# Kernel optimization log

Measured on AMD Instinct MI355X. Metric: run time of the kernel, lower is better.

The kernel has to match this reference:

```python
import jax, jax.numpy as jnp
import numpy as np
import math

PSIZE = [(8, 8), (16, 16)]


def _conv2d(x, w, b):
    # 3x3 stride-1 'SAME' conv, NCHW / OIHW
    y = jax.lax.conv_general_dilated(
        x, w, window_strides=(1, 1), padding='SAME',
        dimension_numbers=('NCHW', 'OIHW', 'NCHW'))
    return y + b[None, :, None, None]


def _patch_attention(x, xs, b, t, c, h, w, ph, pw):
    oh, ow = h // ph, w // pw
    d = c * ph * pw
    # query: [b, oh*ow, c*ph*pw]
    q = x.reshape(b, c, oh, ph, ow, pw).transpose(0, 2, 4, 1, 3, 5).reshape(b, oh * ow, d)
    # key/value: [b, t*oh*ow, c*ph*pw]
    k = xs.reshape(b, t, c, oh, ph, ow, pw).transpose(0, 1, 3, 5, 2, 4, 6).reshape(b, t * oh * ow, d)
    scores = jnp.einsum('bqd,bkd->bqk', q, k) / jnp.asarray(math.sqrt(d), x.dtype)
    # NOTE: the original torch code calls scores.masked_fill(mm, -1e9) without
    # assigning the result, so the mask has NO effect; we faithfully omit it.
    atten = jax.nn.softmax(scores, axis=-1)
    val = jnp.einsum('bqk,bkd->bqd', atten, k)
    y = val.reshape(b, oh, ow, c, ph, pw).transpose(0, 3, 1, 4, 2, 5).reshape(b, c, h, w)
    return y


def setup_inputs() -> dict:
    key = jax.random.key(0)
    ks = jax.random.split(key, 6)
    b, t, c, h, w = 2, 5, 256, 128, 128
    n_p = len(PSIZE)
    x = jax.random.normal(ks[0], (b, c, h, w), dtype=jnp.float32)
    xs = jax.random.normal(ks[1], (b * t, c, h, w), dtype=jnp.float32)
    ms = jax.random.uniform(ks[2], (b * t, 1, h, w), dtype=jnp.float32)
    fan_lin = c * n_p * 9
    w_lin = jax.random.normal(ks[3], (c, c * n_p, 3, 3), dtype=jnp.float32) * (1.0 / math.sqrt(fan_lin))
    b_lin = jnp.zeros((c,), dtype=jnp.float32)
    fan_g = 512 * 9
    w_gate = jax.random.normal(ks[4], (c, 2 * c, 3, 3), dtype=jnp.float32) * (1.0 / math.sqrt(fan_g))
    b_gate = jnp.zeros((c,), dtype=jnp.float32)
    w_feat = jax.random.normal(ks[5], (c, 2 * c, 3, 3), dtype=jnp.float32) * (1.0 / math.sqrt(fan_g))
    b_feat = jnp.zeros((c,), dtype=jnp.float32)
    return {'x': x, 'xs': xs, 'ms': ms, 'w_lin': w_lin, 'b_lin': b_lin,
            'w_gate': w_gate, 'b_gate': b_gate, 'w_feat': w_feat, 'b_feat': b_feat}


def reference(x, xs, ms, w_lin, b_lin, w_gate, b_gate, w_feat, b_feat):
    b, c, h, w = x.shape
    t = xs.shape[0] // b
    outs = [_patch_attention(x, xs, b, t, c, h, w, ph, pw) for (ph, pw) in PSIZE]
    out = jnp.concatenate(outs, axis=1)                    # [b, c*len(psize), h, w]
    out = jax.nn.leaky_relu(_conv2d(out, w_lin, b_lin), 0.2)  # [b, c, h, w]
    fused = jnp.concatenate([x, out], axis=1)              # [b, 2c, h, w]
    gating = _conv2d(fused, w_gate, b_gate)
    feature = jax.nn.leaky_relu(_conv2d(fused, w_feat, b_feat), 0.2)
    x_out = jax.nn.sigmoid(gating) * feature               # [b, c, h, w]
    return x_out
```

## Files before the change

### kernel.cpp

```cpp
#include <hip/hip_runtime.h>

typedef unsigned short u16;
typedef unsigned int u32;
typedef __attribute__((ext_vector_type(8))) short bf16x8;
typedef __attribute__((ext_vector_type(4))) float f32x4;

#define MFMA16(d, a, bb) d = __builtin_amdgcn_mfma_f32_16x16x32_bf16(a, bb, d, 0, 0, 0)

#define PROW 130
#define PIMG 16900
#define PIMGC (16900 * 512)

__device__ __forceinline__ u16 f2bf(float f){
  union { float f; u32 i; } v; v.f = f;
  u32 r = v.i + 0x7fffu + ((v.i >> 16) & 1u);
  return (u16)(r >> 16);
}

__device__ __forceinline__ void gl16(const u16* g, u16* l){
  __builtin_amdgcn_global_load_lds(
      (const __attribute__((address_space(1))) u32*)g,
      (__attribute__((address_space(3))) u32*)l, 16, 0, 0);
}

__global__ __launch_bounds__(256) void k_border(u16* __restrict__ buf){
  const int b = blockIdx.y;
  const int j = blockIdx.x * 4 + (threadIdx.x >> 6);
  const int l = threadIdx.x & 63;
  int pp;
  if(j < 130)       pp = j;
  else if(j < 260)  pp = 129 * 130 + (j - 130);
  else if(j < 388)  pp = (j - 259) * 130;
  else              pp = (j - 387) * 130 + 129;
  u16* p = buf + ((size_t)b * PIMG + pp) * 512 + l * 8;
  *(uint4*)p = (uint4){0u, 0u, 0u, 0u};
}

__global__ __launch_bounds__(256) void k_transpose_pad(const float* __restrict__ in,
                                                       u16* __restrict__ out){
  __shared__ float s[32][33];
  const float* ip = in + (size_t)blockIdx.z * 256 * 16384;
  u16* op = out + (size_t)blockIdx.z * PIMGC;
  int r0 = blockIdx.x * 32, c0 = blockIdx.y * 32;
  int tx = threadIdx.x, ty = threadIdx.y;
#pragma unroll
  for(int i = 0; i < 4; ++i){
    int r = ty * 4 + i;
    s[r][tx] = ip[(size_t)(r0 + r) * 16384 + (c0 + tx)];
  }
  __syncthreads();
#pragma unroll
  for(int i = 0; i < 4; ++i){
    int pix = c0 + ty * 4 + i;
    u32 pp = ((u32)(pix >> 7) + 1) * PROW + (pix & 127) + 1;
    op[(size_t)pp * 512 + (r0 + tx)] = f2bf(s[tx][ty * 4 + i]);
  }
}

__global__ __launch_bounds__(256) void k_transpose(const float* __restrict__ in,
                                                   u16* __restrict__ out,
                                                   int rows, int cols,
                                                   int ostride, size_t o_imgstride){
  __shared__ float s[32][33];
  const float* ip = in + (size_t)blockIdx.z * (size_t)rows * (size_t)cols;
  u16* op = out + (size_t)blockIdx.z * o_imgstride;
  int r0 = blockIdx.x * 32, c0 = blockIdx.y * 32;
  int tx = threadIdx.x, ty = threadIdx.y;
#pragma unroll
  for(int i = 0; i < 4; ++i){
    int r = ty * 4 + i;
    s[r][tx] = ip[(size_t)(r0 + r) * cols + (c0 + tx)];
  }
  __syncthreads();
#pragma unroll
  for(int i = 0; i < 4; ++i){
    int c = ty * 4 + i;
    op[(size_t)(c0 + c) * ostride + (r0 + tx)] = f2bf(s[tx][c]);
  }
}

__global__ __launch_bounds__(256) void k_wt(const float* __restrict__ in,
                                            u16* __restrict__ out,
                                            int co_mul, int co_off, int co_tot){
  int ci = blockIdx.x * 256 + threadIdx.x;
  int co = blockIdx.y;
  int e  = blockIdx.z;
  out[((size_t)e * co_tot + co * co_mul + co_off) * 512 + ci] =
      f2bf(in[((size_t)co * 512 + ci) * 9 + e]);
}

__global__ __launch_bounds__(256) void k_scores8(const u16* __restrict__ FUSEDP,
                                                 const u16* __restrict__ XST,
                                                 float* __restrict__ S8p){
  __shared__ u16 As[4096], Bs[4096];
  const int bz = blockIdx.z, b = bz >> 3, g = bz & 7;
  const int q0 = blockIdx.x * 128, k0 = blockIdx.y * 128;
  const int tid = threadIdx.x, w = tid >> 6, l = tid & 63;
  const int wr = w >> 1, wc = w & 1;
  const int l15 = l & 15, kg = (l >> 4) * 8;
  f32x4 acc[4][4];
#pragma unroll
  for(int m = 0; m < 4; ++m)
#pragma unroll
    for(int n = 0; n < 4; ++n) acc[m][n] = (f32x4){0.f, 0.f, 0.f, 0.f};

  for(int e8 = 0; e8 < 8; ++e8){
    const int e = g * 8 + e8, dy = e >> 3, dx = e & 7;
    for(int ci0 = 0; ci0 < 256; ci0 += 32){
#pragma unroll
      for(int r = 0; r < 2; ++r){
        const int idx = (w * 2 + r) * 64 + l;
        const int q = q0 + (idx >> 2);
        const int apy = ((q >> 4) << 3) + dy, apx = ((q & 15) << 3) + dx;
        const size_t pa = ((size_t)b * PIMG + (size_t)(apy + 1) * PROW + apx + 1) * 512
                          + ci0 + (idx & 3) * 8;
        gl16(FUSEDP + pa, As + (size_t)(w * 2 + r) * 512);
        const int k = k0 + (idx >> 2), t = k >> 8, rm = k & 255;
        const size_t pb = (((size_t)b * 5 + t) * 16384 +
                           (size_t)(((rm >> 4) << 3) + dy) * 128 + ((rm & 15) << 3) + dx) * 256
                          + ci0 + (idx & 3) * 8;
        gl16(XST + pb, Bs + (size_t)(w * 2 + r) * 512);
      }
      __syncthreads();
      bf16x8 af[4], bq[4];
#pragma unroll
      for(int m = 0; m < 4; ++m) af[m] = *(const bf16x8*)(As + (wr * 64 + m * 16 + l15) * 32 + kg);
#pragma unroll
      for(int n = 0; n < 4; ++n) bq[n] = *(const bf16x8*)(Bs + (wc * 64 + n * 16 + l15) * 32 + kg);
#pragma unroll
      for(int m = 0; m < 4; ++m)
#pragma unroll
        for(int n = 0; n < 4; ++n)
          acc[m][n] = __builtin_amdgcn_mfma_f32_16x16x32_bf16(af[m], bq[n], acc[m][n], 0, 0, 0);
      __syncthreads();
    }
  }
  float* dst = S8p + ((size_t)g * 2 + b) * 256 * 1280;
#pragma unroll
  for(int m = 0; m < 4; ++m){
    const int q = q0 + wr * 64 + m * 16 + (l >> 4) * 4;
#pragma unroll
    for(int n = 0; n < 4; ++n){
      const int k = k0 + wc * 64 + n * 16 + l15;
#pragma unroll
      for(int r = 0; r < 4; ++r) dst[(size_t)(q + r) * 1280 + k] = acc[m][n][r];
    }
  }
}

__global__ __launch_bounds__(256) void k_softmax8(const float* __restrict__ S8p,
                                                  u16* __restrict__ A8){
  __shared__ float red[8];
  int b = blockIdx.x >> 8, q = blockIdx.x & 255;
  size_t roff = ((size_t)b * 256 + q) * 1280;
  int tid = threadIdx.x;
  float v[5]; float m = -1e30f;
#pragma unroll
  for(int i = 0; i < 5; ++i){
    size_t o = roff + tid + 256 * i;
    float s = 0.f;
#pragma unroll
    for(int g = 0; g < 8; ++g) s += S8p[(size_t)g * 655360 + o];
    v[i] = s * 0.0078125f; m = fmaxf(m, v[i]);
  }
#pragma unroll
  for(int o = 32; o > 0; o >>= 1) m = fmaxf(m, __shfl_xor(m, o));
  int wid = tid >> 6;
  if((tid & 63) == 0) red[wid] = m;
  __syncthreads();
  m = fmaxf(fmaxf(red[0], red[1]), fmaxf(red[2], red[3]));
  float s = 0.f;
#pragma unroll
  for(int i = 0; i < 5; ++i){ v[i] = __expf(v[i] - m); s += v[i]; }
#pragma unroll
  for(int o = 32; o > 0; o >>= 1) s += __shfl_xor(s, o);
  if((tid & 63) == 0) red[4 + wid] = s;
  __syncthreads();
  s = red[4] + red[5] + red[6] + red[7];
  float inv = 1.0f / s;
#pragma unroll
  for(int i = 0; i < 5; ++i) A8[roff + tid + 256 * i] = f2bf(v[i] * inv);
}

__global__ __launch_bounds__(320) void k_s16(const float* __restrict__ S8p,
                                             u16* __restrict__ A16){
  __shared__ float red[10];
  int b = blockIdx.x >> 6, q16 = blockIdx.x & 63;
  int tid = threadIdx.x;
  int t = tid >> 6, rm = tid & 63;
  int KY = rm >> 3, KX = rm & 7;
  int QY = q16 >> 3, QX = q16 & 7;
  float s = 0.f;
#pragma unroll
  for(int i = 0; i < 2; ++i)
#pragma unroll
    for(int j = 0; j < 2; ++j){
      int q8 = (2 * QY + i) * 16 + (2 * QX + j);
      int k8 = t * 256 + (2 * KY + i) * 16 + (2 * KX + j);
      size_t o = ((size_t)b * 256 + q8) * 1280 + k8;
#pragma unroll
      for(int g = 0; g < 8; ++g) s += S8p[(size_t)g * 655360 + o];
    }
  s *= 0.00390625f;
  float m = s;
#pragma unroll
  for(int o = 32; o > 0; o >>= 1) m = fmaxf(m, __shfl_xor(m, o));
  int wid = tid >> 6;
  if((tid & 63) == 0) red[wid] = m;
  __syncthreads();
  m = fmaxf(fmaxf(fmaxf(red[0], red[1]), fmaxf(red[2], red[3])), red[4]);
  float e = __expf(s - m);
  float sm = e;
#pragma unroll
  for(int o = 32; o > 0; o >>= 1) sm += __shfl_xor(sm, o);
  if((tid & 63) == 0) red[5 + wid] = sm;
  __syncthreads();
  sm = red[5] + red[6] + red[7] + red[8] + red[9];
  A16[((size_t)b * 64 + q16) * 320 + tid] = f2bf(e / sm);
}

__global__ __launch_bounds__(256) void k_val8(const u16* __restrict__ A8,
                                              const u16* __restrict__ XST,
                                              u16* __restrict__ OUTCATP){
  __shared__ u16 As[4096];
  __shared__ u16 Bs[128 * 40];
  const int z = blockIdx.z, b = z >> 6, rr = z & 63;
  const int ry = rr >> 3, rx = rr & 7;
  const int q0 = blockIdx.x * 128, c0 = blockIdx.y * 128;
  const int tid = threadIdx.x, w = tid >> 6, l = tid & 63;
  const int wr = w >> 1, wc = w & 1;
  const int l15 = l & 15, kg = (l >> 4) * 8;
  const int k2 = tid >> 4, ch8 = tid & 15;
  f32x4 acc[4][4];
#pragma unroll
  for(int m = 0; m < 4; ++m)
#pragma unroll
    for(int n = 0; n < 4; ++n) acc[m][n] = (f32x4){0.f, 0.f, 0.f, 0.f};

  for(int k0 = 0; k0 < 1280; k0 += 32){
#pragma unroll
    for(int r = 0; r < 2; ++r){
      const int idx = (w * 2 + r) * 64 + l;
      const u16* ga = A8 + ((size_t)b * 256 + q0 + (idx >> 2)) * 1280 + k0 + (idx & 3) * 8;
      gl16(ga, As + (size_t)(w * 2 + r) * 512);
    }
    {
      const int ka = k0 + k2 * 2, kb = ka + 1;
      const int ta = ka >> 8, ra = ka & 255;
      const int tb = kb >> 8, rb = kb & 255;
      const size_t pa = (((size_t)b * 5 + ta) * 16384 +
                         (size_t)(((ra >> 4) << 3) + ry) * 128 + ((ra & 15) << 3) + rx) * 256
                        + c0 + ch8 * 8;
      const size_t pb = (((size_t)b * 5 + tb) * 16384 +
                         (size_t)(((rb >> 4) << 3) + ry) * 128 + ((rb & 15) << 3) + rx) * 256
                        + c0 + ch8 * 8;
      union { uint4 v; u16 s[8]; } u0, u1;
      u0.v = *(const uint4*)(XST + pa);
      u1.v = *(const uint4*)(XST + pb);
      const int kloc = k2 * 2, swz = (ch8 & 3) << 3;
#pragma unroll
      for(int j = 0; j < 8; ++j){
        u32 pack = (u32)u0.s[j] | ((u32)u1.s[j] << 16);
        *(u32*)(Bs + (size_t)(ch8 * 8 + j) * 40 + (kloc ^ swz)) = pack;
      }
    }
    __syncthreads();
    bf16x8 af[4], bq[4];
#pragma unroll
    for(int m = 0; m < 4; ++m) af[m] = *(const bf16x8*)(As + (wr * 64 + m * 16 + l15) * 32 + kg);
#pragma unroll
    for(int n = 0; n < 4; ++n){
      const int ch = wc * 64 + n * 16 + l15;
      bq[n] = *(const bf16x8*)(Bs + (size_t)ch * 40 + (kg ^ (((ch >> 3) & 3) << 3)));
    }
#pragma unroll
    for(int m = 0; m < 4; ++m)
#pragma unroll
      for(int n = 0; n < 4; ++n)
        acc[m][n] = __builtin_amdgcn_mfma_f32_16x16x32_bf16(af[m], bq[n], acc[m][n], 0, 0, 0);
    __syncthreads();
  }
#pragma unroll
  for(int m = 0; m < 4; ++m){
    const int qb = q0 + wr * 64 + m * 16 + (l >> 4) * 4;
#pragma unroll
    for(int n = 0; n < 4; ++n){
      const int ch = c0 + wc * 64 + n * 16 + l15;
#pragma unroll
      for(int r = 0; r < 4; ++r){
        const int q = qb + r;
        const int py = ((q >> 4) << 3) + ry, px = ((q & 15) << 3) + rx;
        OUTCATP[((size_t)b * PIMG + (size_t)(py + 1) * PROW + px + 1) * 512 + ch] = f2bf(acc[m][n][r]);
      }
    }
  }
}

__global__ __launch_bounds__(256) void k_val16(const u16* __restrict__ A16,
                                               const u16* __restrict__ XST,
                                               u16* __restrict__ OUTCATP){
  __shared__ u16 As[64 * 32];
  __shared__ u16 Bs[128 * 40];
  const int z = blockIdx.z, b = z >> 8, rr = z & 255;
  const int ry = rr >> 4, rx = rr & 15;
  const int c0 = blockIdx.y * 128;
  const int tid = threadIdx.x, w = tid >> 6, l = tid & 63;
  const int l15 = l & 15, kg = (l >> 4) * 8;
  const int k2 = tid >> 4, ch8 = tid & 15;
  f32x4 acc[4][2];
#pragma unroll
  for(int m = 0; m < 4; ++m)
#pragma unroll
    for(int n = 0; n < 2; ++n) acc[m][n] = (f32x4){0.f, 0.f, 0.f, 0.f};

  for(int k0 = 0; k0 < 320; k0 += 32){
    {
      const int idx = w * 64 + l;
      const u16* ga = A16 + ((size_t)b * 64 + (idx >> 2)) * 320 + k0 + (idx & 3) * 8;
      gl16(ga, As + (size_t)w * 512);
    }
    {
      const int ka = k0 + k2 * 2, kb = ka + 1;
      const int ta = ka >> 6, ra = ka & 63;
      const int tb = kb >> 6, rb = kb & 63;
      const size_t pa = (((size_t)b * 5 + ta) * 16384 +
                         (size_t)(((ra >> 3) << 4) + ry) * 128 + ((ra & 7) << 4) + rx) * 256
                        + c0 + ch8 * 8;
      const size_t pb = (((size_t)b * 5 + tb) * 16384 +
                         (size_t)(((rb >> 3) << 4) + ry) * 128 + ((rb & 7) << 4) + rx) * 256
                        + c0 + ch8 * 8;
      union { uint4 v; u16 s[8]; } u0, u1;
      u0.v = *(const uint4*)(XST + pa);
      u1.v = *(const uint4*)(XST + pb);
      const int kloc = k2 * 2, swz = (ch8 & 3) << 3;
#pragma unroll
      for(int j = 0; j < 8; ++j){
        u32 pack = (u32)u0.s[j] | ((u32)u1.s[j] << 16);
        *(u32*)(Bs + (size_t)(ch8 * 8 + j) * 40 + (kloc ^ swz)) = pack;
      }
    }
    __syncthreads();
    bf16x8 af[4], bq[2];
#pragma unroll
    for(int m = 0; m < 4; ++m) af[m] = *(const bf16x8*)(As + (m * 16 + l15) * 32 + kg);
#pragma unroll
    for(int n = 0; n < 2; ++n){
      const int ch = w * 32 + n * 16 + l15;
      bq[n] = *(const bf16x8*)(Bs + (size_t)ch * 40 + (kg ^ (((ch >> 3) & 3) << 3)));
    }
#pragma unroll
    for(int m = 0; m < 4; ++m)
#pragma unroll
      for(int n = 0; n < 2; ++n)
        acc[m][n] = __builtin_amdgcn_mfma_f32_16x16x32_bf16(af[m], bq[n], acc[m][n], 0, 0, 0);
    __syncthreads();
  }
#pragma unroll
  for(int m = 0; m < 4; ++m){
    const int qb = m * 16 + (l >> 4) * 4;
#pragma unroll
    for(int n = 0; n < 2; ++n){
      const int ch = c0 + w * 32 + n * 16 + l15;
#pragma unroll
      for(int r = 0; r < 4; ++r){
        const int q = qb + r;
        const int py = ((q >> 3) << 4) + ry, px = ((q & 7) << 4) + rx;
        OUTCATP[((size_t)b * PIMG + (size_t)(py + 1) * PROW + px + 1) * 512 + 256 + ch] = f2bf(acc[m][n][r]);
      }
    }
  }
}

__global__ __launch_bounds__(512, 4) void k_convA(const u16* __restrict__ A,
                                                  const u16* __restrict__ W,
                                                  const float* __restrict__ bias,
                                                  u16* __restrict__ FUSEDP){
  constexpr int NT = 72;
  __shared__ u16 lds[2][16384];
  const int id = blockIdx.x;
  const int wg = (id & 7) * 64 + (id >> 3);
  const int mt = wg & 127, rest = wg >> 7;
  const int n0 = (rest & 1) * 128, b = rest >> 1;
  const int m0 = mt * 128;
  const int tid = threadIdx.x, w = tid >> 6, l = tid & 63;
  const int wr = w >> 2, wc = w & 3;
  const int l15 = l & 15, lq = l >> 4;
  const int lr = l >> 3;
  const u32 laneswz = (u32)((((l & 7) * 16) ^ (lr << 4)) >> 1);

  u32 aB[2], bB[2];
#pragma unroll
  for(int j = 0; j < 2; ++j){
    const int row = (w * 2 + j) * 8 + lr;
    const int p = m0 + row;
    aB[j] = ((u32)b * PIMG + ((u32)(p >> 7) + 1) * PROW + (u32)(p & 127) + 1) * 512 + laneswz;
    bB[j] = (u32)(n0 + row) * 512 + laneswz;
  }

  f32x4 acc[4][2];
#pragma unroll
  for(int m = 0; m < 4; ++m)
#pragma unroll
    for(int n = 0; n < 2; ++n) acc[m][n] = (f32x4){0.f, 0.f, 0.f, 0.f};

  auto STAGE = [&](int kt){
    const int e = kt % 9, ci0 = (kt / 9) << 6;
    const int dy = e / 3 - 1, dx = e % 3 - 1;
    const int aD = (dy * PROW + dx) * 512 + ci0;
    const u32 bD = (u32)e * 256u * 512u + ci0;
    u16* bufA = &lds[kt & 1][0];
    u16* bufB = &lds[kt & 1][8192];
#pragma unroll
    for(int j = 0; j < 2; ++j){
      const int c = w * 2 + j;
      gl16(A + aB[j] + aD, bufA + c * 512);
      gl16(W + bB[j] + bD, bufB + c * 512);
    }
  };

  STAGE(0);
  STAGE(1);

  for(int t = 0; t < NT; ++t){
    if(t < NT - 1) asm volatile("s_waitcnt vmcnt(4)" ::: "memory");
    else           asm volatile("s_waitcnt vmcnt(0)" ::: "memory");
    __builtin_amdgcn_s_barrier();
    const char* bufA = (const char*)&lds[t & 1][0];
    const char* bufB = bufA + 16384;
    bf16x8 af[4][2], bq[2][2];
#pragma unroll
    for(int m = 0; m < 4; ++m){
      const int row = wr * 64 + m * 16 + l15;
      const int sz = (row & 7) << 4;
#pragma unroll
      for(int kk = 0; kk < 2; ++kk)
        af[m][kk] = *(const bf16x8*)(bufA + row * 128 + (((kk * 4 + lq) * 16) ^ sz));
    }
#pragma unroll
    for(int n = 0; n < 2; ++n){
      const int row = wc * 32 + n * 16 + l15;
      const int sz = (row & 7) << 4;
#pragma unroll
      for(int kk = 0; kk < 2; ++kk)
        bq[n][kk] = *(const bf16x8*)(bufB + row * 128 + (((kk * 4 + lq) * 16) ^ sz));
    }
    asm volatile("s_waitcnt lgkmcnt(0)" ::: "memory");
    __builtin_amdgcn_sched_barrier(0);
    __builtin_amdgcn_s_barrier();
    if(t + 2 < NT) STAGE(t + 2);
    __builtin_amdgcn_s_setprio(1);
#pragma unroll
    for(int kk = 0; kk < 2; ++kk)
#pragma unroll
      for(int m = 0; m < 4; ++m)
#pragma unroll
        for(int n = 0; n < 2; ++n)
          MFMA16(acc[m][n], af[m][kk], bq[n][kk]);
    __builtin_amdgcn_s_setprio(0);
  }

#pragma unroll
  for(int m = 0; m < 4; ++m){
    const int p0 = m0 + wr * 64 + m * 16 + lq * 4;
    const size_t pp = ((size_t)b * PIMG + (size_t)((p0 >> 7) + 1) * PROW + (p0 & 127) + 1) * 512;
#pragma unroll
    for(int n = 0; n < 2; ++n){
      const int co = n0 + wc * 32 + n * 16 + l15;
      const float bi = bias[co];
#pragma unroll
      for(int r = 0; r < 4; ++r){
        float v = acc[m][n][r] + bi;
        v = v > 0.f ? v : 0.2f * v;
        FUSEDP[pp + (size_t)r * 512 + 256 + co] = f2bf(v);
      }
    }
  }
}

__global__ __launch_bounds__(512, 2) void k_convB(const u16* __restrict__ A,
                                                  const u16* __restrict__ W,
                                                  const float* __restrict__ bias,
                                                  const float* __restrict__ bias2,
                                                  float* __restrict__ out){
  constexpr int NT = 72;
  __shared__ u16 lds[2][32768];
  const int id = blockIdx.x;
  const int wg = (id & 7) * 32 + (id >> 3);
  const int mt = wg & 63, rest = wg >> 6;
  const int n0 = (rest & 1) * 256, b = rest >> 1;
  const int m0 = mt * 256;
  const int tid = threadIdx.x, w = tid >> 6, l = tid & 63;
  const int wr = w >> 2, wc = w & 3;
  const int l15 = l & 15, lq = l >> 4;
  const int lr = l >> 3;
  const u32 laneswz = (u32)((((l & 7) * 16) ^ (lr << 4)) >> 1);

  u32 aB[2][2], bB[2][2];
#pragma unroll
  for(int half = 0; half < 2; ++half)
#pragma unroll
    for(int j = 0; j < 2; ++j){
      const int row = half * 128 + (w * 2 + j) * 8 + lr;
      const int p = m0 + row;
      aB[half][j] = ((u32)b * PIMG + ((u32)(p >> 7) + 1) * PROW + (u32)(p & 127) + 1) * 512 + laneswz;
      bB[half][j] = (u32)(n0 + row) * 512 + laneswz;
    }

  f32x4 acc[8][4];
#pragma unroll
  for(int m = 0; m < 8; ++m)
#pragma unroll
    for(int n = 0; n < 4; ++n) acc[m][n] = (f32x4){0.f, 0.f, 0.f, 0.f};

  auto STAGE_A = [&](int kt, int half){
    const int e = kt % 9, ci0 = (kt / 9) << 6;
    const int dy = e / 3 - 1, dx = e % 3 - 1;
    const int aD = (dy * PROW + dx) * 512 + ci0;
    u16* dstbase = &lds[kt & 1][0];
#pragma unroll
    for(int j = 0; j < 2; ++j){
      const int rowc = half * 128 + (w * 2 + j) * 8;
      gl16(A + aB[half][j] + aD, dstbase + rowc * 64);
    }
  };
  auto STAGE_B = [&](int kt, int half){
    const int e = kt % 9, ci0 = (kt / 9) << 6;
    const u32 bD = (u32)e * 512u * 512u + ci0;
    u16* dstbase = &lds[kt & 1][16384];
#pragma unroll
    for(int j = 0; j < 2; ++j){
      const int rowc = half * 128 + (w * 2 + j) * 8;
      gl16(W + bB[half][j] + bD, dstbase + rowc * 64);
    }
  };

  STAGE_B(0, 0); STAGE_B(0, 1); STAGE_A(0, 0); STAGE_A(0, 1);
  STAGE_B(1, 0); STAGE_B(1, 1); STAGE_A(1, 0);
  asm volatile("s_waitcnt vmcnt(6)" ::: "memory");
  __builtin_amdgcn_s_barrier();

  for(int t = 0; t < NT; ++t){
    const char* bufA = (const char*)&lds[t & 1][0];
    const char* bufB = bufA + 32768;
    bf16x8 af[8], bq0[4], bq1[4];
#pragma unroll
    for(int m = 0; m < 8; ++m){
      const int row = wr * 128 + m * 16 + l15;
      af[m] = *(const bf16x8*)(bufA + row * 128 + ((lq * 16) ^ ((row & 7) << 4)));
    }
#pragma unroll
    for(int n = 0; n < 4; ++n){
      const int row = wc * 64 + n * 16 + l15;
      const int sz = (row & 7) << 4;
      bq0[n] = *(const bf16x8*)(bufB + row * 128 + ((lq * 16) ^ sz));
      bq1[n] = *(const bf16x8*)(bufB + row * 128 + ((64 + lq * 16) ^ sz));
    }
    if(t + 1 < NT) STAGE_A(t + 1, 1);
    asm volatile("s_waitcnt lgkmcnt(0)" ::: "memory");
    __builtin_amdgcn_sched_barrier(0);
    __builtin_amdgcn_s_setprio(1);
#pragma unroll
    for(int m = 0; m < 8; ++m){
      MFMA16(acc[m][0], af[m], bq0[0]);
      MFMA16(acc[m][1], af[m], bq0[1]);
    }
    __builtin_amdgcn_s_setprio(0);
    __builtin_amdgcn_s_barrier();
    if(t + 2 < NT) STAGE_B(t + 2, 0);
    __builtin_amdgcn_s_setprio(1);
#pragma unroll
    for(int m = 0; m < 8; ++m){
      MFMA16(acc[m][2], af[m], bq0[2]);
      MFMA16(acc[m][3], af[m], bq0[3]);
    }
    __builtin_amdgcn_s_setprio(0);
    __builtin_amdgcn_s_barrier();
#pragma unroll
    for(int m = 0; m < 8; ++m){
      const int row = wr * 128 + m * 16 + l15;
      af[m] = *(const bf16x8*)(bufA + row * 128 + ((64 + lq * 16) ^ ((row & 7) << 4)));
    }
    if(t + 2 < NT) STAGE_B(t + 2, 1);
    asm volatile("s_waitcnt lgkmcnt(0)" ::: "memory");
    __builtin_amdgcn_sched_barrier(0);
    __builtin_amdgcn_s_setprio(1);
#pragma unroll
    for(int m = 0; m < 8; ++m){
      MFMA16(acc[m][0], af[m], bq1[0]);
      MFMA16(acc[m][1], af[m], bq1[1]);
    }
    __builtin_amdgcn_s_setprio(0);
    __builtin_amdgcn_s_barrier();
    if(t + 2 < NT) STAGE_A(t + 2, 0);
    __builtin_amdgcn_s_setprio(1);
#pragma unroll
    for(int m = 0; m < 8; ++m){
      MFMA16(acc[m][2], af[m], bq1[2]);
      MFMA16(acc[m][3], af[m], bq1[3]);
    }
    __builtin_amdgcn_s_setprio(0);
    if(t < NT - 2){
      asm volatile("s_waitcnt vmcnt(6)" ::: "memory");
    } else if(t == NT - 2){
      asm volatile("s_waitcnt vmcnt(0)" ::: "memory");
    }
    __builtin_amdgcn_s_barrier();
  }

#pragma unroll
  for(int m = 0; m < 8; ++m){
    const int p0 = m0 + wr * 128 + m * 16 + lq * 4;
#pragma unroll
    for(int n = 0; n < 4; ++n){
      const int col = n0 + wc * 64 + n * 16 + l15;
      const int s = col & 1, co = col >> 1;
      const float big = bias[co], bif = bias2[co];
      float res[4];
#pragma unroll
      for(int r = 0; r < 4; ++r){
        const float val = acc[m][n][r];
        const float oth = __shfl_xor(val, 1);
        float gg = s ? oth : val;
        float ff = s ? val : oth;
        gg += big; ff += bif;
        ff = ff > 0.f ? ff : 0.2f * ff;
        res[r] = ff / (1.0f + __expf(-gg));
      }
      if(s == 0){
        float4 v4 = make_float4(res[0], res[1], res[2], res[3]);
        *(float4*)&out[((size_t)b * 256 + co) * 16384 + p0] = v4;
      }
    }
  }
}

extern "C" void kernel_launch(void* const* d_in, const int* in_sizes, int n_in,
                              void* d_out, int out_size, void* d_ws, size_t ws_size,
                              hipStream_t stream){
  const float* x      = (const float*)d_in[0];
  const float* xs     = (const float*)d_in[1];
  const float* w_lin  = (const float*)d_in[3];
  const float* b_lin  = (const float*)d_in[4];
  const float* w_gate = (const float*)d_in[5];
  const float* b_gate = (const float*)d_in[6];
  const float* w_feat = (const float*)d_in[7];
  const float* b_feat = (const float*)d_in[8];
  float* out = (float*)d_out;

  char* ws = (char*)d_ws;
  size_t off = 0;
  auto alloc = [&](size_t bytes) -> void* {
    void* p = ws + off;
    off += (bytes + 255) & ~(size_t)255;
    return p;
  };
  u16* FUSEDP  = (u16*)alloc(2ull * PIMGC * 2);
  u16* OUTCATP = (u16*)alloc(2ull * PIMGC * 2);
  u16* XST     = (u16*)alloc(10ull * 16384 * 256 * 2);
  u16* WTl     = (u16*)alloc(9ull * 256 * 512 * 2);
  u16* WGF     = (u16*)alloc(9ull * 512 * 512 * 2);
  float* S8p   = (float*)alloc(8ull * 655360 * 4);
  u16* A8      = (u16*)alloc(655360ull * 2);
  u16* A16     = (u16*)alloc(2ull * 64 * 320 * 2);

  k_border<<<dim3(129, 2), 256, 0, stream>>>(FUSEDP);
  k_border<<<dim3(129, 2), 256, 0, stream>>>(OUTCATP);

  dim3 tb(32, 8);
  k_transpose_pad<<<dim3(8, 512, 2), tb, 0, stream>>>(x, FUSEDP);
  k_transpose<<<dim3(8, 512, 10), tb, 0, stream>>>(xs, XST, 256, 16384, 256, 4194304ull);

  k_wt<<<dim3(2, 256, 9), 256, 0, stream>>>(w_lin,  WTl, 1, 0, 256);
  k_wt<<<dim3(2, 256, 9), 256, 0, stream>>>(w_gate, WGF, 2, 0, 512);
  k_wt<<<dim3(2, 256, 9), 256, 0, stream>>>(w_feat, WGF, 2, 1, 512);

  k_scores8<<<dim3(2, 10, 16), 256, 0, stream>>>(FUSEDP, XST, S8p);
  k_softmax8<<<512, 256, 0, stream>>>(S8p, A8);
  k_s16<<<128, 320, 0, stream>>>(S8p, A16);

  k_val8 <<<dim3(2, 2, 128), 256, 0, stream>>>(A8, XST, OUTCATP);
  k_val16<<<dim3(1, 2, 512), 256, 0, stream>>>(A16, XST, OUTCATP);

  k_convA<<<512, 512, 0, stream>>>(OUTCATP, WTl, b_lin, FUSEDP);
  k_convB<<<256, 512, 0, stream>>>(FUSEDP, WGF, b_gate, b_feat, out);
}
```

Baseline: 406.5 us.

## Unify conv kernels into templated K=32 pipeline with smaller tiles for convB

Replaces the two separate implicit-GEMM conv kernels with one templated kernel that stages K in 32-channel slices (144 steps) instead of 64, with a new 4-row swizzle. The gate/feature conv now uses 128x256 tiles with 512 blocks and occupancy 4 instead of 256x256 tiles with 256 blocks and occupancy 2. The aim is less LDS per block, more resident waves and better latency hiding. In exchange there are twice as many barriers and pipeline steps, and less operand reuse per LDS load.

```diff
diff --git a/kernel.cpp b/kernel.cpp
--- a/kernel.cpp
+++ b/kernel.cpp
@@ -371,78 +371,86 @@
   }
 }
 
-__global__ __launch_bounds__(512, 4) void k_convA(const u16* __restrict__ A,
-                                                  const u16* __restrict__ W,
-                                                  const float* __restrict__ bias,
-                                                  u16* __restrict__ FUSEDP){
-  constexpr int NT = 72;
-  __shared__ u16 lds[2][16384];
+__device__ __forceinline__ int swz32(int row){
+  return ((row ^ (row >> 2)) & 3) << 4;
+}
+
+template<int MODE>
+__global__ __launch_bounds__(512, 4) void k_conv32(const u16* __restrict__ A,
+                                                   const u16* __restrict__ W,
+                                                   const float* __restrict__ bias,
+                                                   const float* __restrict__ bias2,
+                                                   void* __restrict__ outp){
+  constexpr int NT   = 144;
+  constexpr int BN   = (MODE == 0) ? 128 : 256;
+  constexpr int NF   = BN / 64;
+  constexpr int NTOT = (MODE == 0) ? 256 : 512;
+  constexpr int BJ   = BN / 128;
+  constexpr int BUFU = (128 + BN) * 32;
+  __shared__ u16 lds[2][BUFU];
   const int id = blockIdx.x;
   const int wg = (id & 7) * 64 + (id >> 3);
-  const int mt = wg & 127, rest = wg >> 7;
-  const int n0 = (rest & 1) * 128, b = rest >> 1;
-  const int m0 = mt * 128;
+  const int ntile = wg >> 8;
+  const int mm = wg & 255, b = mm >> 7, mt = mm & 127;
+  const int m0 = mt * 128, n0 = ntile * BN;
   const int tid = threadIdx.x, w = tid >> 6, l = tid & 63;
   const int wr = w >> 2, wc = w & 3;
   const int l15 = l & 15, lq = l >> 4;
-  const int lr = l >> 3;
-  const u32 laneswz = (u32)((((l & 7) * 16) ^ (lr << 4)) >> 1);
-
-  u32 aB[2], bB[2];
-#pragma unroll
-  for(int j = 0; j < 2; ++j){
-    const int row = (w * 2 + j) * 8 + lr;
+
+  const int srow = l >> 2;
+  const u32 lanec = (u32)((((l & 3) * 16) ^ swz32(srow)) >> 1);
+
+  u32 aB, bB[BJ];
+  {
+    const int row = w * 16 + srow;
     const int p = m0 + row;
-    aB[j] = ((u32)b * PIMG + ((u32)(p >> 7) + 1) * PROW + (u32)(p & 127) + 1) * 512 + laneswz;
-    bB[j] = (u32)(n0 + row) * 512 + laneswz;
-  }
-
-  f32x4 acc[4][2];
+    aB = ((u32)b * PIMG + ((u32)(p >> 7) + 1) * PROW + (u32)(p & 127) + 1) * 512 + lanec;
+#pragma unroll
+    for(int j = 0; j < BJ; ++j){
+      const int rowb = (w * BJ + j) * 16 + srow;
+      bB[j] = (u32)(n0 + rowb) * 512 + lanec;
+    }
+  }
+
+  f32x4 acc[4][NF];
 #pragma unroll
   for(int m = 0; m < 4; ++m)
 #pragma unroll
-    for(int n = 0; n < 2; ++n) acc[m][n] = (f32x4){0.f, 0.f, 0.f, 0.f};
+    for(int n = 0; n < NF; ++n) acc[m][n] = (f32x4){0.f, 0.f, 0.f, 0.f};
 
   auto STAGE = [&](int kt){
-    const int e = kt % 9, ci0 = (kt / 9) << 6;
+    const int g = kt / 18, sub = kt % 18;
+    const int e = sub % 9, ci0 = g * 64 + (sub / 9) * 32;
     const int dy = e / 3 - 1, dx = e % 3 - 1;
     const int aD = (dy * PROW + dx) * 512 + ci0;
-    const u32 bD = (u32)e * 256u * 512u + ci0;
+    const u32 bD = (u32)e * NTOT * 512u + ci0;
     u16* bufA = &lds[kt & 1][0];
-    u16* bufB = &lds[kt & 1][8192];
-#pragma unroll
-    for(int j = 0; j < 2; ++j){
-      const int c = w * 2 + j;
-      gl16(A + aB[j] + aD, bufA + c * 512);
-      gl16(W + bB[j] + bD, bufB + c * 512);
-    }
+    u16* bufB = &lds[kt & 1][4096];
+    gl16(A + aB + aD, bufA + w * 512);
+#pragma unroll
+    for(int j = 0; j < BJ; ++j)
+      gl16(W + bB[j] + bD, bufB + (w * BJ + j) * 512);
   };
 
   STAGE(0);
   STAGE(1);
 
   for(int t = 0; t < NT; ++t){
-    if(t < NT - 1) asm volatile("s_waitcnt vmcnt(4)" ::: "memory");
+    if(t < NT - 1) asm volatile("s_waitcnt vmcnt(%0)" :: "i"(1 + BJ) : "memory");
     else           asm volatile("s_waitcnt vmcnt(0)" ::: "memory");
     __builtin_amdgcn_s_barrier();
     const char* bufA = (const char*)&lds[t & 1][0];
-    const char* bufB = bufA + 16384;
-    bf16x8 af[4][2], bq[2][2];
+    const char* bufB = bufA + 8192;
+    bf16x8 af[4], bq[NF];
 #pragma unroll
     for(int m = 0; m < 4; ++m){
       const int row = wr * 64 + m * 16 + l15;
-      const int sz = (row & 7) << 4;
-#pragma unroll
-      for(int kk = 0; kk < 2; ++kk)
-        af[m][kk] = *(const bf16x8*)(bufA + row * 128 + (((kk * 4 + lq) * 16) ^ sz));
-    }
-#pragma unroll
-    for(int n = 0; n < 2; ++n){
-      const int row = wc * 32 + n * 16 + l15;
-      const int sz = (row & 7) << 4;
-#pragma unroll
-      for(int kk = 0; kk < 2; ++kk)
-        bq[n][kk] = *(const bf16x8*)(bufB + row * 128 + (((kk * 4 + lq) * 16) ^ sz));
+      af[m] = *(const bf16x8*)(bufA + row * 64 + ((lq * 16) ^ swz32(row)));
+    }
+#pragma unroll
+    for(int n = 0; n < NF; ++n){
+      const int row = wc * (BN / 4) + n * 16 + l15;
+      bq[n] = *(const bf16x8*)(bufB + row * 64 + ((lq * 16) ^ swz32(row)));
     }
     asm volatile("s_waitcnt lgkmcnt(0)" ::: "memory");
     __builtin_amdgcn_sched_barrier(0);
@@ -450,185 +458,56 @@
     if(t + 2 < NT) STAGE(t + 2);
     __builtin_amdgcn_s_setprio(1);
 #pragma unroll
-    for(int kk = 0; kk < 2; ++kk)
-#pragma unroll
-      for(int m = 0; m < 4; ++m)
-#pragma unroll
-        for(int n = 0; n < 2; ++n)
-          MFMA16(acc[m][n], af[m][kk], bq[n][kk]);
+    for(int m = 0; m < 4; ++m)
+#pragma unroll
+      for(int n = 0; n < NF; ++n)
+        MFMA16(acc[m][n], af[m], bq[n]);
     __builtin_amdgcn_s_setprio(0);
   }
 
-#pragma unroll
-  for(int m = 0; m < 4; ++m){
-    const int p0 = m0 + wr * 64 + m * 16 + lq * 4;
-    const size_t pp = ((size_t)b * PIMG + (size_t)((p0 >> 7) + 1) * PROW + (p0 & 127) + 1) * 512;
-#pragma unroll
-    for(int n = 0; n < 2; ++n){
-      const int co = n0 + wc * 32 + n * 16 + l15;
-      const float bi = bias[co];
-#pragma unroll
-      for(int r = 0; r < 4; ++r){
-        float v = acc[m][n][r] + bi;
-        v = v > 0.f ? v : 0.2f * v;
-        FUSEDP[pp + (size_t)r * 512 + 256 + co] = f2bf(v);
-      }
-    }
-  }
-}
-
-__global__ __launch_bounds__(512, 2) void k_convB(const u16* __restrict__ A,
-                                                  const u16* __restrict__ W,
-                                                  const float* __restrict__ bias,
-                                                  const float* __restrict__ bias2,
-                                                  float* __restrict__ out){
-  constexpr int NT = 72;
-  __shared__ u16 lds[2][32768];
-  const int id = blockIdx.x;
-  const int wg = (id & 7) * 32 + (id >> 3);
-  const int mt = wg & 63, rest = wg >> 6;
-  const int n0 = (rest & 1) * 256, b = rest >> 1;
-  const int m0 = mt * 256;
-  const int tid = threadIdx.x, w = tid >> 6, l = tid & 63;
-  const int wr = w >> 2, wc = w & 3;
-  const int l15 = l & 15, lq = l >> 4;
-  const int lr = l >> 3;
-  const u32 laneswz = (u32)((((l & 7) * 16) ^ (lr << 4)) >> 1);
-
-  u32 aB[2][2], bB[2][2];
-#pragma unroll
-  for(int half = 0; half < 2; ++half)
-#pragma unroll
-    for(int j = 0; j < 2; ++j){
-      const int row = half * 128 + (w * 2 + j) * 8 + lr;
-      const int p = m0 + row;
-      aB[half][j] = ((u32)b * PIMG + ((u32)(p >> 7) + 1) * PROW + (u32)(p & 127) + 1) * 512 + laneswz;
-      bB[half][j] = (u32)(n0 + row) * 512 + laneswz;
-    }
-
-  f32x4 acc[8][4];
-#pragma unroll
-  for(int m = 0; m < 8; ++m)
-#pragma unroll
-    for(int n = 0; n < 4; ++n) acc[m][n] = (f32x4){0.f, 0.f, 0.f, 0.f};
-
-  auto STAGE_A = [&](int kt, int half){
-    const int e = kt % 9, ci0 = (kt / 9) << 6;
-    const int dy = e / 3 - 1, dx = e % 3 - 1;
-    const int aD = (dy * PROW + dx) * 512 + ci0;
-    u16* dstbase = &lds[kt & 1][0];
-#pragma unroll
-    for(int j = 0; j < 2; ++j){
-      const int rowc = half * 128 + (w * 2 + j) * 8;
-      gl16(A + aB[half][j] + aD, dstbase + rowc * 64);
-    }
-  };
-  auto STAGE_B = [&](int kt, int half){
-    const int e = kt % 9, ci0 = (kt / 9) << 6;
-    const u32 bD = (u32)e * 512u * 512u + ci0;
-    u16* dstbase = &lds[kt & 1][16384];
-#pragma unroll
-    for(int j = 0; j < 2; ++j){
-      const int rowc = half * 128 + (w * 2 + j) * 8;
-      gl16(W + bB[half][j] + bD, dstbase + rowc * 64);
-    }
-  };
-
-  STAGE_B(0, 0); STAGE_B(0, 1); STAGE_A(0, 0); STAGE_A(0, 1);
-  STAGE_B(1, 0); STAGE_B(1, 1); STAGE_A(1, 0);
-  asm volatile("s_waitcnt vmcnt(6)" ::: "memory");
-  __builtin_amdgcn_s_barrier();
-
-  for(int t = 0; t < NT; ++t){
-    const char* bufA = (const char*)&lds[t & 1][0];
-    const char* bufB = bufA + 32768;
-    bf16x8 af[8], bq0[4], bq1[4];
-#pragma unroll
-    for(int m = 0; m < 8; ++m){
-      const int row = wr * 128 + m * 16 + l15;
-      af[m] = *(const bf16x8*)(bufA + row * 128 + ((lq * 16) ^ ((row & 7) << 4)));
-    }
-#pragma unroll
-    for(int n = 0; n < 4; ++n){
-      const int row = wc * 64 + n * 16 + l15;
-      const int sz = (row & 7) << 4;
-      bq0[n] = *(const bf16x8*)(bufB + row * 128 + ((lq * 16) ^ sz));
-      bq1[n] = *(const bf16x8*)(bufB + row * 128 + ((64 + lq * 16) ^ sz));
-    }
-    if(t + 1 < NT) STAGE_A(t + 1, 1);
-    asm volatile("s_waitcnt lgkmcnt(0)" ::: "memory");
-    __builtin_amdgcn_sched_barrier(0);
-    __builtin_amdgcn_s_setprio(1);
-#pragma unroll
-    for(int m = 0; m < 8; ++m){
-      MFMA16(acc[m][0], af[m], bq0[0]);
-      MFMA16(acc[m][1], af[m], bq0[1]);
-    }
-    __builtin_amdgcn_s_setprio(0);
-    __builtin_amdgcn_s_barrier();
-    if(t + 2 < NT) STAGE_B(t + 2, 0);
-    __builtin_amdgcn_s_setprio(1);
-#pragma unroll
-    for(int m = 0; m < 8; ++m){
-      MFMA16(acc[m][2], af[m], bq0[2]);
-      MFMA16(acc[m][3], af[m], bq0[3]);
-    }
-    __builtin_amdgcn_s_setprio(0);
-    __builtin_amdgcn_s_barrier();
-#pragma unroll
-    for(int m = 0; m < 8; ++m){
-      const int row = wr * 128 + m * 16 + l15;
-      af[m] = *(const bf16x8*)(bufA + row * 128 + ((64 + lq * 16) ^ ((row & 7) << 4)));
-    }
-    if(t + 2 < NT) STAGE_B(t + 2, 1);
-    asm volatile("s_waitcnt lgkmcnt(0)" ::: "memory");
-    __builtin_amdgcn_sched_barrier(0);
-    __builtin_amdgcn_s_setprio(1);
-#pragma unroll
-    for(int m = 0; m < 8; ++m){
-      MFMA16(acc[m][0], af[m], bq1[0]);
-      MFMA16(acc[m][1], af[m], bq1[1]);
-    }
-    __builtin_amdgcn_s_setprio(0);
-    __builtin_amdgcn_s_barrier();
-    if(t + 2 < NT) STAGE_A(t + 2, 0);
-    __builtin_amdgcn_s_setprio(1);
-#pragma unroll
-    for(int m = 0; m < 8; ++m){
-      MFMA16(acc[m][2], af[m], bq1[2]);
-      MFMA16(acc[m][3], af[m], bq1[3]);
-    }
-    __builtin_amdgcn_s_setprio(0);
-    if(t < NT - 2){
-      asm volatile("s_waitcnt vmcnt(6)" ::: "memory");
-    } else if(t == NT - 2){
-      asm volatile("s_waitcnt vmcnt(0)" ::: "memory");
-    }
-    __builtin_amdgcn_s_barrier();
-  }
-
-#pragma unroll
-  for(int m = 0; m < 8; ++m){
-    const int p0 = m0 + wr * 128 + m * 16 + lq * 4;
-#pragma unroll
-    for(int n = 0; n < 4; ++n){
-      const int col = n0 + wc * 64 + n * 16 + l15;
-      const int s = col & 1, co = col >> 1;
-      const float big = bias[co], bif = bias2[co];
-      float res[4];
-#pragma unroll
-      for(int r = 0; r < 4; ++r){
-        const float val = acc[m][n][r];
-        const float oth = __shfl_xor(val, 1);
-        float gg = s ? oth : val;
-        float ff = s ? val : oth;
-        gg += big; ff += bif;
-        ff = ff > 0.f ? ff : 0.2f * ff;
-        res[r] = ff / (1.0f + __expf(-gg));
-      }
-      if(s == 0){
-        float4 v4 = make_float4(res[0], res[1], res[2], res[3]);
-        *(float4*)&out[((size_t)b * 256 + co) * 16384 + p0] = v4;
+  if(MODE == 0){
+    u16* ob = (u16*)outp;
+#pragma unroll
+    for(int m = 0; m < 4; ++m){
+      const int p0 = m0 + wr * 64 + m * 16 + lq * 4;
+      const size_t pp = ((size_t)b * PIMG + (size_t)((p0 >> 7) + 1) * PROW + (p0 & 127) + 1) * 512;
+#pragma unroll
+      for(int n = 0; n < NF; ++n){
+        const int co = n0 + wc * 32 + n * 16 + l15;
+        const float bi = bias[co];
+#pragma unroll
+        for(int r = 0; r < 4; ++r){
+          float v = acc[m][n][r] + bi;
+          v = v > 0.f ? v : 0.2f * v;
+          ob[pp + (size_t)r * 512 + 256 + co] = f2bf(v);
+        }
+      }
+    }
+  } else {
+    float* ob = (float*)outp;
+#pragma unroll
+    for(int m = 0; m < 4; ++m){
+      const int p0 = m0 + wr * 64 + m * 16 + lq * 4;
+#pragma unroll
+      for(int n = 0; n < NF; ++n){
+        const int col = n0 + wc * 64 + n * 16 + l15;
+        const int s = col & 1, co = col >> 1;
+        const float big = bias[co], bif = bias2[co];
+        float res[4];
+#pragma unroll
+        for(int r = 0; r < 4; ++r){
+          const float val = acc[m][n][r];
+          const float oth = __shfl_xor(val, 1);
+          float gg = s ? oth : val;
+          float ff = s ? val : oth;
+          gg += big; ff += bif;
+          ff = ff > 0.f ? ff : 0.2f * ff;
+          res[r] = ff / (1.0f + __expf(-gg));
+        }
+        if(s == 0){
+          float4 v4 = make_float4(res[0], res[1], res[2], res[3]);
+          *(float4*)&ob[((size_t)b * 256 + co) * 16384 + p0] = v4;
+        }
       }
     }
   }
@@ -681,6 +560,6 @@
   k_val8 <<<dim3(2, 2, 128), 256, 0, stream>>>(A8, XST, OUTCATP);
   k_val16<<<dim3(1, 2, 512), 256, 0, stream>>>(A16, XST, OUTCATP);
 
-  k_convA<<<512, 512, 0, stream>>>(OUTCATP, WTl, b_lin, FUSEDP);
-  k_convB<<<256, 512, 0, stream>>>(FUSEDP, WGF, b_gate, b_feat, out);
-}
+  k_conv32<0><<<512, 512, 0, stream>>>(OUTCATP, WTl, b_lin, nullptr, (void*)FUSEDP);
+  k_conv32<1><<<512, 512, 0, stream>>>(FUSEDP, WGF, b_gate, b_feat, (void*)out);
+}
```

Result: slower. 447.6 us (+10.1%).

## Split gate/feature conv tile across 16 waves with simpler double-buffer pipeline

Applied to the files above, without the earlier changes.

Rewrites the fused gate/feature 3x3 conv GEMM kernel to run 1024-thread blocks (16 waves) on the same 256x256 output tile. Each wave now owns a 64x64 sub-tile instead of 128x64, which halves its accumulator registers. The staging of A and B is merged into a single per-iteration prefetch two k-steps ahead, with one wait and barrier per step. The aim is more waves to hide memory and LDS latency. The cost is tighter register budgets from the launch bounds, which may cause spills, and a coarser overlap of global loads with MFMA work.

```diff
diff --git a/kernel.cpp b/kernel.cpp
--- a/kernel.cpp
+++ b/kernel.cpp
@@ -477,139 +477,109 @@
   }
 }
 
-__global__ __launch_bounds__(512, 2) void k_convB(const u16* __restrict__ A,
-                                                  const u16* __restrict__ W,
-                                                  const float* __restrict__ bias,
-                                                  const float* __restrict__ bias2,
-                                                  float* __restrict__ out){
+__global__ __launch_bounds__(1024, 4) void k_convB16(const u16* __restrict__ A,
+                                                     const u16* __restrict__ W,
+                                                     const float* __restrict__ bias,
+                                                     const float* __restrict__ bias2,
+                                                     float* __restrict__ out){
   constexpr int NT = 72;
   __shared__ u16 lds[2][32768];
   const int id = blockIdx.x;
   const int wg = (id & 7) * 32 + (id >> 3);
-  const int mt = wg & 63, rest = wg >> 6;
-  const int n0 = (rest & 1) * 256, b = rest >> 1;
-  const int m0 = mt * 256;
+  const int ntile = wg >> 7;
+  const int rem = wg & 127, b = rem >> 6, mt = rem & 63;
+  const int m0 = mt * 256, n0 = ntile * 256;
   const int tid = threadIdx.x, w = tid >> 6, l = tid & 63;
   const int wr = w >> 2, wc = w & 3;
   const int l15 = l & 15, lq = l >> 4;
   const int lr = l >> 3;
   const u32 laneswz = (u32)((((l & 7) * 16) ^ (lr << 4)) >> 1);
 
-  u32 aB[2][2], bB[2][2];
-#pragma unroll
-  for(int half = 0; half < 2; ++half)
-#pragma unroll
-    for(int j = 0; j < 2; ++j){
-      const int row = half * 128 + (w * 2 + j) * 8 + lr;
-      const int p = m0 + row;
-      aB[half][j] = ((u32)b * PIMG + ((u32)(p >> 7) + 1) * PROW + (u32)(p & 127) + 1) * 512 + laneswz;
-      bB[half][j] = (u32)(n0 + row) * 512 + laneswz;
-    }
-
-  f32x4 acc[8][4];
-#pragma unroll
-  for(int m = 0; m < 8; ++m)
+  u32 aB[2], bB[2];
+#pragma unroll
+  for(int j = 0; j < 2; ++j){
+    const int row = (w * 2 + j) * 8 + lr;
+    const int p = m0 + row;
+    aB[j] = ((u32)b * PIMG + ((u32)(p >> 7) + 1) * PROW + (u32)(p & 127) + 1) * 512 + laneswz;
+    bB[j] = (u32)(n0 + row) * 512 + laneswz;
+  }
+
+  f32x4 acc[4][4];
+#pragma unroll
+  for(int m = 0; m < 4; ++m)
 #pragma unroll
     for(int n = 0; n < 4; ++n) acc[m][n] = (f32x4){0.f, 0.f, 0.f, 0.f};
 
-  auto STAGE_A = [&](int kt, int half){
+  auto STAGE = [&](int kt){
     const int e = kt % 9, ci0 = (kt / 9) << 6;
     const int dy = e / 3 - 1, dx = e % 3 - 1;
     const int aD = (dy * PROW + dx) * 512 + ci0;
-    u16* dstbase = &lds[kt & 1][0];
+    const u32 bD = (u32)e * 512u * 512u + ci0;
+    u16* bufA = &lds[kt & 1][0];
+    u16* bufB = &lds[kt & 1][16384];
 #pragma unroll
     for(int j = 0; j < 2; ++j){
-      const int rowc = half * 128 + (w * 2 + j) * 8;
-      gl16(A + aB[half][j] + aD, dstbase + rowc * 64);
+      const int c = w * 2 + j;
+      gl16(A + aB[j] + aD, bufA + c * 512);
+      gl16(W + bB[j] + bD, bufB + c * 512);
     }
   };
-  auto STAGE_B = [&](int kt, int half){
-    const int e = kt % 9, ci0 = (kt / 9) << 6;
-    const u32 bD = (u32)e * 512u * 512u + ci0;
-    u16* dstbase = &lds[kt & 1][16384];
-#pragma unroll
-    for(int j = 0; j < 2; ++j){
-      const int rowc = half * 128 + (w * 2 + j) * 8;
-      gl16(W + bB[half][j] + bD, dstbase + rowc * 64);
-    }
-  };
-
-  STAGE_B(0, 0); STAGE_B(0, 1); STAGE_A(0, 0); STAGE_A(0, 1);
-  STAGE_B(1, 0); STAGE_B(1, 1); STAGE_A(1, 0);
-  asm volatile("s_waitcnt vmcnt(6)" ::: "memory");
-  __builtin_amdgcn_s_barrier();
+
+  STAGE(0);
+  STAGE(1);
 
   for(int t = 0; t < NT; ++t){
+    if(t < NT - 1) asm volatile("s_waitcnt vmcnt(4)" ::: "memory");
+    else           asm volatile("s_waitcnt vmcnt(0)" ::: "memory");
+    __builtin_amdgcn_s_barrier();
     const char* bufA = (const char*)&lds[t & 1][0];
     const char* bufB = bufA + 32768;
-    bf16x8 af[8], bq0[4], bq1[4];
-#pragma unroll
-    for(int m = 0; m < 8; ++m){
-      const int row = wr * 128 + m * 16 + l15;
+    bf16x8 af[4], bq[4];
+#pragma unroll
+    for(int m = 0; m < 4; ++m){
+      const int row = wr * 64 + m * 16 + l15;
       af[m] = *(const bf16x8*)(bufA + row * 128 + ((lq * 16) ^ ((row & 7) << 4)));
     }
 #pragma unroll
     for(int n = 0; n < 4; ++n){
       const int row = wc * 64 + n * 16 + l15;
-      const int sz = (row & 7) << 4;
-      bq0[n] = *(const bf16x8*)(bufB + row * 128 + ((lq * 16) ^ sz));
-      bq1[n] = *(const bf16x8*)(bufB + row * 128 + ((64 + lq * 16) ^ sz));
-    }
-    if(t + 1 < NT) STAGE_A(t + 1, 1);
+      bq[n] = *(const bf16x8*)(bufB + row * 128 + ((lq * 16) ^ ((row & 7) << 4)));
+    }
     asm volatile("s_waitcnt lgkmcnt(0)" ::: "memory");
     __builtin_amdgcn_sched_barrier(0);
     __builtin_amdgcn_s_setprio(1);
 #pragma unroll
-    for(int m = 0; m < 8; ++m){
-      MFMA16(acc[m][0], af[m], bq0[0]);
-      MFMA16(acc[m][1], af[m], bq0[1]);
-    }
+    for(int m = 0; m < 4; ++m)
+#pragma unroll
+      for(int n = 0; n < 4; ++n)
+        MFMA16(acc[m][n], af[m], bq[n]);
     __builtin_amdgcn_s_setprio(0);
-    __builtin_amdgcn_s_barrier();
-    if(t + 2 < NT) STAGE_B(t + 2, 0);
-    __builtin_amdgcn_s_setprio(1);
-#pragma unroll
-    for(int m = 0; m < 8; ++m){
-      MFMA16(acc[m][2], af[m], bq0[2]);
-      MFMA16(acc[m][3], af[m], bq0[3]);
-    }
-    __builtin_amdgcn_s_setprio(0);
-    __builtin_amdgcn_s_barrier();
-#pragma unroll
-    for(int m = 0; m < 8; ++m){
-      const int row = wr * 128 + m * 16 + l15;
+#pragma unroll
+    for(int m = 0; m < 4; ++m){
+      const int row = wr * 64 + m * 16 + l15;
       af[m] = *(const bf16x8*)(bufA + row * 128 + ((64 + lq * 16) ^ ((row & 7) << 4)));
     }
-    if(t + 2 < NT) STAGE_B(t + 2, 1);
+#pragma unroll
+    for(int n = 0; n < 4; ++n){
+      const int row = wc * 64 + n * 16 + l15;
+      bq[n] = *(const bf16x8*)(bufB + row * 128 + ((64 + lq * 16) ^ ((row & 7) << 4)));
+    }
     asm volatile("s_waitcnt lgkmcnt(0)" ::: "memory");
     __builtin_amdgcn_sched_barrier(0);
+    __builtin_amdgcn_s_barrier();
+    if(t + 2 < NT) STAGE(t + 2);
     __builtin_amdgcn_s_setprio(1);
 #pragma unroll
-    for(int m = 0; m < 8; ++m){
-      MFMA16(acc[m][0], af[m], bq1[0]);
-      MFMA16(acc[m][1], af[m], bq1[1]);
-    }
+    for(int m = 0; m < 4; ++m)
+#pragma unroll
+      for(int n = 0; n < 4; ++n)
+        MFMA16(acc[m][n], af[m], bq[n]);
     __builtin_amdgcn_s_setprio(0);
-    __builtin_amdgcn_s_barrier();
-    if(t + 2 < NT) STAGE_A(t + 2, 0);
-    __builtin_amdgcn_s_setprio(1);
-#pragma unroll
-    for(int m = 0; m < 8; ++m){
-      MFMA16(acc[m][2], af[m], bq1[2]);
-      MFMA16(acc[m][3], af[m], bq1[3]);
-    }
-    __builtin_amdgcn_s_setprio(0);
-    if(t < NT - 2){
-      asm volatile("s_waitcnt vmcnt(6)" ::: "memory");
-    } else if(t == NT - 2){
-      asm volatile("s_waitcnt vmcnt(0)" ::: "memory");
-    }
-    __builtin_amdgcn_s_barrier();
-  }
-
-#pragma unroll
-  for(int m = 0; m < 8; ++m){
-    const int p0 = m0 + wr * 128 + m * 16 + lq * 4;
+  }
+
+#pragma unroll
+  for(int m = 0; m < 4; ++m){
+    const int p0 = m0 + wr * 64 + m * 16 + lq * 4;
 #pragma unroll
     for(int n = 0; n < 4; ++n){
       const int col = n0 + wc * 64 + n * 16 + l15;
@@ -682,5 +652,5 @@
   k_val16<<<dim3(1, 2, 512), 256, 0, stream>>>(A16, XST, OUTCATP);
 
   k_convA<<<512, 512, 0, stream>>>(OUTCATP, WTl, b_lin, FUSEDP);
-  k_convB<<<256, 512, 0, stream>>>(FUSEDP, WGF, b_gate, b_feat, out);
-}
+  k_convB16<<<256, 1024, 0, stream>>>(FUSEDP, WGF, b_gate, b_feat, out);
+}
```

After: 405.2 us. No clear change (-0.3%).
